# Performance work log

Measured on AMD Instinct MI355X. Metric: run time of the kernel, lower is better.

The kernel has to match this reference:

```python
import jax, jax.numpy as jnp
import numpy as np

B, S, T, D_IN = 32, 64, 30, 500  # batch, outer seq, LSTM time steps, LSTM input size
L = 64  # stacked LSTM layers, hidden_size = 1


def setup_inputs() -> dict:
    key = jax.random.key(0)
    ks = jax.random.split(key, 9)
    s = 0.2  # param scale ~ uniform(-1,1) stddev regime of torch init (1/sqrt(hidden)=1)
    return {
        "x": jax.random.normal(ks[0], (B, S, T * D_IN), jnp.float32),
        "w_ih0": jax.random.normal(ks[1], (4, D_IN), jnp.float32) * s,
        "w_hh0": jax.random.normal(ks[2], (4, 1), jnp.float32) * s,
        "b_ih0": jax.random.normal(ks[3], (4,), jnp.float32) * s,
        "b_hh0": jax.random.normal(ks[4], (4,), jnp.float32) * s,
        "w_ih": jax.random.normal(ks[5], (L - 1, 4, 1), jnp.float32) * s,
        "w_hh": jax.random.normal(ks[6], (L - 1, 4, 1), jnp.float32) * s,
        "b_ih": jax.random.normal(ks[7], (L - 1, 4), jnp.float32) * s,
        "b_hh": jax.random.normal(ks[8], (L - 1, 4), jnp.float32) * s,
    }


def _scan_layer(pre, whh):
    """Run one hidden-width-1 LSTM layer. pre: (T, N, 4) input-side gate preacts
    (incl. both biases); whh: (4,) recurrent weights. Returns hidden stream (T, N)."""
    N = pre.shape[1]
    z = jnp.zeros((N,), pre.dtype)

    def cell(carry, g_in):
        h, c = carry
        g = g_in + h[:, None] * whh  # (N, 4), torch gate order i,f,g,o
        i = jax.nn.sigmoid(g[:, 0])
        f = jax.nn.sigmoid(g[:, 1])
        gg = jnp.tanh(g[:, 2])
        o = jax.nn.sigmoid(g[:, 3])
        c = f * c + i * gg
        h = o * jnp.tanh(c)
        return (h, c), h

    _, hs = jax.lax.scan(cell, (z, z), pre)
    return hs  # (T, N)


def reference(x, w_ih0, w_hh0, b_ih0, b_hh0, w_ih, w_hh, b_ih, b_hh):
    b, s, d = x.shape
    xf = jnp.flip(x, -1).reshape(b * s, T, D_IN)  # (N, T, 500)
    # layer 0: precompute input contribution for all timesteps (the only GEMM)
    pre0 = jnp.einsum('ntd,gd->tng', xf, w_ih0) + b_ih0 + b_hh0  # (T, N, 4)
    hs = _scan_layer(pre0, w_hh0[:, 0])  # (T, N)

    # layers 1..63: scalar-input LSTMs, scanned over the layer axis
    def layer_step(seq, params):
        wih, whh, bias = params  # (4,), (4,), (4,)
        pre = seq[:, :, None] * wih + bias  # (T, N, 4)
        return _scan_layer(pre, whh), None

    hs, _ = jax.lax.scan(layer_step, hs, (w_ih[:, :, 0], w_hh[:, :, 0], b_ih + b_hh))
    return hs.transpose(1, 0).reshape(b, s, T)  # (B, S, 30)
```

## Files before the change

### kernel.cpp

```cpp
#include <hip/hip_runtime.h>

#define NSEQ 2048
#define TT 30
#define DIN 500
#define NLAYER 64

__device__ __forceinline__ float fexp(float x) {
    return __builtin_amdgcn_exp2f(x * 1.4426950408889634f);
}
__device__ __forceinline__ float fsigmoid(float x) {
    return __builtin_amdgcn_rcpf(1.0f + fexp(-x));
}
__device__ __forceinline__ float ftanh_(float x) {
    return fmaf(-2.0f, __builtin_amdgcn_rcpf(1.0f + fexp(2.0f * x)), 1.0f);
}
__device__ __forceinline__ float rdlane(float v, int l) {
    return __builtin_bit_cast(float, __builtin_amdgcn_readlane(__builtin_bit_cast(int, v), l));
}
template <int CTRL>
__device__ __forceinline__ float dppmv(float v) {
    return __builtin_bit_cast(float, __builtin_amdgcn_update_dpp(
        0, __builtin_bit_cast(int, v), CTRL, 0xF, 0xF, false));
}
#define DPP_XOR1 0xB1
#define DPP_XOR2 0x4E
#define DPP_ROR4 0x124
#define DPP_ROR8 0x128
#define DPP_SHR1 0x138

__device__ __forceinline__ float dot4rev(const float4 xv, const float4 wv, float acc) {
    acc = fmaf(xv.x, wv.w, acc);
    acc = fmaf(xv.y, wv.z, acc);
    acc = fmaf(xv.z, wv.y, acc);
    acc = fmaf(xv.w, wv.x, acc);
    return acc;
}
__device__ __forceinline__ float red16(float a) {
    a += dppmv<DPP_XOR1>(a);
    a += dppmv<DPP_XOR2>(a);
    a += dppmv<DPP_ROR4>(a);
    a += dppmv<DPP_ROR8>(a);
    return a;
}

__global__ __launch_bounds__(256, 2) void fused_lstm(
    const float* __restrict__ x,
    const float* __restrict__ w_ih0,
    const float* __restrict__ w_hh0,
    const float* __restrict__ b_ih0,
    const float* __restrict__ b_hh0,
    const float* __restrict__ w_ih,
    const float* __restrict__ w_hh,
    const float* __restrict__ b_ih,
    const float* __restrict__ b_hh,
    float* __restrict__ out)
{
    __shared__ float pre[4][TT * 4];

    const int tid  = threadIdx.x;
    const int lane = tid & 63;
    const int w    = tid >> 6;
    const int n    = blockIdx.x * 4 + w;
    const int s    = lane & 15;
    const int g    = lane >> 4;
    float* __restrict__ prew = pre[w];

    const int l = (lane == 0) ? 0 : (lane - 1);
    float4 wihv  = *(const float4*)(w_ih + l * 4);
    float4 whhv  = *(const float4*)(w_hh + l * 4);
    float4 bihv  = *(const float4*)(b_ih + l * 4);
    float4 bhhv  = *(const float4*)(b_hh + l * 4);
    float4 whh0v = *(const float4*)(w_hh0);
    float4 bi0v  = *(const float4*)(b_ih0);
    float4 bh0v  = *(const float4*)(b_hh0);
    __builtin_amdgcn_sched_barrier(0);

    const float4* __restrict__ w4 = (const float4*)w_ih0;
    const float4 z4 = make_float4(0.f, 0.f, 0.f, 0.f);
    float4 wk[4][8];
#pragma unroll
    for (int gate = 0; gate < 4; ++gate) {
#pragma unroll
        for (int k = 0; k < 8; ++k) {
            const int j = k * 16 + s;
            wk[gate][k] = (j < 125) ? w4[gate * 125 + (124 - j)] : z4;
        }
    }

    const float4* __restrict__ xq = (const float4*)(x + (size_t)n * (TT * DIN));
    auto xround = [&](int r, float4 (&b)[8]) {
        const int t = r * 4 + g;
        int cc = TT - 1 - t; if (cc < 0) cc = 0;
        const float4* __restrict__ p = xq + cc * 125;
#pragma unroll
        for (int k = 0; k < 8; ++k) {
            const int j = k * 16 + s;
            b[k] = p[(j < 125) ? j : 124];
        }
    };
    auto cround = [&](const float4 (&b)[8], int r) {
        float a0 = 0.f, a1 = 0.f, a2 = 0.f, a3 = 0.f;
#pragma unroll
        for (int k = 0; k < 8; ++k) {
            a0 = dot4rev(b[k], wk[0][k], a0);
            a1 = dot4rev(b[k], wk[1][k], a1);
            a2 = dot4rev(b[k], wk[2][k], a2);
            a3 = dot4rev(b[k], wk[3][k], a3);
        }
        a0 = red16(a0); a1 = red16(a1); a2 = red16(a2); a3 = red16(a3);
        const int t = r * 4 + g;
        if (s == 0 && t < TT)
            *(float4*)&prew[t * 4] = make_float4(a0, a1, a2, a3);
    };

    float4 A[8], B[8];
    xround(0, A);
#pragma unroll
    for (int r = 0; r < 8; r += 2) {
        if (r + 1 < 8) xround(r + 1, B);
        __builtin_amdgcn_sched_barrier(0);
        cround(A, r);
        if (r + 2 < 8) xround(r + 2, A);
        __builtin_amdgcn_sched_barrier(0);
        cround(B, r + 1);
    }
    asm volatile("s_waitcnt lgkmcnt(0)" ::: "memory");

    float wih0, wih1, wih2, wih3, whh0, whh1, whh2, whh3;
    float bia0, bia1, bia2, bia3;
    if (lane == 0) {
        wih0 = wih1 = wih2 = wih3 = 0.f;
        bia0 = bia1 = bia2 = bia3 = 0.f;
        whh0 = whh0v.x; whh1 = whh0v.y; whh2 = whh0v.z; whh3 = whh0v.w;
    } else {
        wih0 = wihv.x; wih1 = wihv.y; wih2 = wihv.z; wih3 = wihv.w;
        whh0 = whhv.x; whh1 = whhv.y; whh2 = whhv.z; whh3 = whhv.w;
        bia0 = bihv.x + bhhv.x; bia1 = bihv.y + bhhv.y;
        bia2 = bihv.z + bhhv.z; bia3 = bihv.w + bhhv.w;
    }
    float pg0 = 0.f, pg1 = 0.f, pg2 = 0.f, pg3 = 0.f;
    if (lane < TT) {
        const float4 q = *(const float4*)&prew[lane * 4];
        pg0 = q.x + bi0v.x + bh0v.x;
        pg1 = q.y + bi0v.y + bh0v.y;
        pg2 = q.z + bi0v.z + bh0v.z;
        pg3 = q.w + bi0v.w + bh0v.w;
    }

    float h = 0.f, c = 0.f;
    for (int k = 0; k < NLAYER + TT - 1; ++k) {
        const float h_in = dppmv<DPP_SHR1>(h);
        const int t = k - lane;
        const bool active = (t >= 0) && (t < TT);

        float g0, g1, g2, g3;
        if (lane == 0) {
            g0 = g1 = g2 = g3 = 0.f;
        } else {
            g0 = fmaf(h_in, wih0, bia0);
            g1 = fmaf(h_in, wih1, bia1);
            g2 = fmaf(h_in, wih2, bia2);
            g3 = fmaf(h_in, wih3, bia3);
        }
        if (k < TT) {
            const float p0 = rdlane(pg0, k);
            const float p1 = rdlane(pg1, k);
            const float p2 = rdlane(pg2, k);
            const float p3 = rdlane(pg3, k);
            if (lane == 0) { g0 = p0; g1 = p1; g2 = p2; g3 = p3; }
        }
        g0 = fmaf(h, whh0, g0);
        g1 = fmaf(h, whh1, g1);
        g2 = fmaf(h, whh2, g2);
        g3 = fmaf(h, whh3, g3);

        const float ig = fsigmoid(g0);
        const float fg = fsigmoid(g1);
        const float gg = ftanh_(g2);
        const float og = fsigmoid(g3);
        const float cn = fmaf(fg, c, ig * gg);
        const float hn = og * ftanh_(cn);

        if (active) { c = cn; h = hn; }
        if (lane == 63 && active) out[(size_t)n * TT + t] = hn;
    }
}

extern "C" void kernel_launch(void* const* d_in, const int* in_sizes, int n_in,
                              void* d_out, int out_size, void* d_ws, size_t ws_size,
                              hipStream_t stream) {
    const float* x     = (const float*)d_in[0];
    const float* w_ih0 = (const float*)d_in[1];
    const float* w_hh0 = (const float*)d_in[2];
    const float* b_ih0 = (const float*)d_in[3];
    const float* b_hh0 = (const float*)d_in[4];
    const float* w_ih  = (const float*)d_in[5];
    const float* w_hh  = (const float*)d_in[6];
    const float* b_ih  = (const float*)d_in[7];
    const float* b_hh  = (const float*)d_in[8];
    float* out = (float*)d_out;

    fused_lstm<<<NSEQ / 4, 256, 0, stream>>>(x, w_ih0, w_hh0, b_ih0, b_hh0,
                                             w_ih, w_hh, b_ih, b_hh, out);
}
```

Baseline: 42.11 us.

## Split fused LSTM into separate GEMV kernel and recurrence kernel via workspace

Splits the fused kernel in two. The first kernel computes the layer-0 input projection with one block per sequence: each wave covers 8 timesteps, holds weights in fewer registers, uses a full-wave DPP reduction, and can run more blocks per CU. Its gate preactivations go to a global workspace, and a second kernel reads them back for the wavefront-skewed recurrence. This gives the memory-bound GEMV more parallelism and frees the recurrence kernel from holding weight registers, at the cost of an extra launch and a global write/read round trip.

```diff
diff --git a/kernel.cpp b/kernel.cpp
--- a/kernel.cpp
+++ b/kernel.cpp
@@ -22,11 +22,13 @@
     return __builtin_bit_cast(float, __builtin_amdgcn_update_dpp(
         0, __builtin_bit_cast(int, v), CTRL, 0xF, 0xF, false));
 }
-#define DPP_XOR1 0xB1
-#define DPP_XOR2 0x4E
-#define DPP_ROR4 0x124
-#define DPP_ROR8 0x128
-#define DPP_SHR1 0x138
+#define DPP_ROW_SHR1   0x111
+#define DPP_ROW_SHR2   0x112
+#define DPP_ROW_SHR4   0x114
+#define DPP_ROW_SHR8   0x118
+#define DPP_BCAST15    0x142
+#define DPP_BCAST31    0x143
+#define DPP_SHR1       0x138
 
 __device__ __forceinline__ float dot4rev(const float4 xv, const float4 wv, float acc) {
     acc = fmaf(xv.x, wv.w, acc);
@@ -35,17 +37,68 @@
     acc = fmaf(xv.w, wv.x, acc);
     return acc;
 }
-__device__ __forceinline__ float red16(float a) {
-    a += dppmv<DPP_XOR1>(a);
-    a += dppmv<DPP_XOR2>(a);
-    a += dppmv<DPP_ROR4>(a);
-    a += dppmv<DPP_ROR8>(a);
+__device__ __forceinline__ float red64(float a) {
+    a += dppmv<DPP_ROW_SHR1>(a);
+    a += dppmv<DPP_ROW_SHR2>(a);
+    a += dppmv<DPP_ROW_SHR4>(a);
+    a += dppmv<DPP_ROW_SHR8>(a);
+    a += dppmv<DPP_BCAST15>(a);
+    a += dppmv<DPP_BCAST31>(a);
     return a;
 }
 
-__global__ __launch_bounds__(256, 2) void fused_lstm(
+__global__ __launch_bounds__(256, 4) void lstm_gemv(
     const float* __restrict__ x,
     const float* __restrict__ w_ih0,
+    float4* __restrict__ preg)
+{
+    const int tid  = threadIdx.x;
+    const int lane = tid & 63;
+    const int w    = tid >> 6;
+    const int n    = blockIdx.x;
+
+    const float4* __restrict__ w4 = (const float4*)w_ih0;
+    const float4 z4 = make_float4(0.f, 0.f, 0.f, 0.f);
+    float4 wq0[4], wq1[4];
+#pragma unroll
+    for (int g = 0; g < 4; ++g) {
+        wq0[g] = w4[g * 125 + (124 - lane)];
+        wq1[g] = (lane < 61) ? w4[g * 125 + (60 - lane)] : z4;
+    }
+
+    const float4* __restrict__ xq = (const float4*)(x + (size_t)n * (TT * DIN));
+    const int xb_idx = (lane < 61) ? (64 + lane) : 124;
+
+    float4 xa[8], xb[8];
+    auto issue = [&](int i) {
+        const int t = 8 * w + i;
+        if (t < TT) {
+            const float4* __restrict__ p = xq + (TT - 1 - t) * 125;
+            xa[i] = p[lane];
+            xb[i] = p[xb_idx];
+        }
+    };
+    issue(0); issue(1); issue(2);
+    __builtin_amdgcn_sched_barrier(0);
+#pragma unroll
+    for (int i = 0; i < 8; ++i) {
+        if (i + 3 < 8) issue(i + 3);
+        __builtin_amdgcn_sched_barrier(0);
+        const int t = 8 * w + i;
+        if (t < TT) {
+            float a0 = dot4rev(xa[i], wq0[0], 0.f); a0 = dot4rev(xb[i], wq1[0], a0);
+            float a1 = dot4rev(xa[i], wq0[1], 0.f); a1 = dot4rev(xb[i], wq1[1], a1);
+            float a2 = dot4rev(xa[i], wq0[2], 0.f); a2 = dot4rev(xb[i], wq1[2], a2);
+            float a3 = dot4rev(xa[i], wq0[3], 0.f); a3 = dot4rev(xb[i], wq1[3], a3);
+            a0 = red64(a0); a1 = red64(a1); a2 = red64(a2); a3 = red64(a3);
+            if (lane == 63) preg[n * TT + t] = make_float4(a0, a1, a2, a3);
+        }
+        __builtin_amdgcn_sched_barrier(0);
+    }
+}
+
+__global__ __launch_bounds__(256, 2) void lstm_rec(
+    const float4* __restrict__ preg,
     const float* __restrict__ w_hh0,
     const float* __restrict__ b_ih0,
     const float* __restrict__ b_hh0,
@@ -55,76 +108,19 @@
     const float* __restrict__ b_hh,
     float* __restrict__ out)
 {
-    __shared__ float pre[4][TT * 4];
-
     const int tid  = threadIdx.x;
     const int lane = tid & 63;
     const int w    = tid >> 6;
     const int n    = blockIdx.x * 4 + w;
-    const int s    = lane & 15;
-    const int g    = lane >> 4;
-    float* __restrict__ prew = pre[w];
 
     const int l = (lane == 0) ? 0 : (lane - 1);
-    float4 wihv  = *(const float4*)(w_ih + l * 4);
-    float4 whhv  = *(const float4*)(w_hh + l * 4);
-    float4 bihv  = *(const float4*)(b_ih + l * 4);
-    float4 bhhv  = *(const float4*)(b_hh + l * 4);
-    float4 whh0v = *(const float4*)(w_hh0);
-    float4 bi0v  = *(const float4*)(b_ih0);
-    float4 bh0v  = *(const float4*)(b_hh0);
-    __builtin_amdgcn_sched_barrier(0);
-
-    const float4* __restrict__ w4 = (const float4*)w_ih0;
-    const float4 z4 = make_float4(0.f, 0.f, 0.f, 0.f);
-    float4 wk[4][8];
-#pragma unroll
-    for (int gate = 0; gate < 4; ++gate) {
-#pragma unroll
-        for (int k = 0; k < 8; ++k) {
-            const int j = k * 16 + s;
-            wk[gate][k] = (j < 125) ? w4[gate * 125 + (124 - j)] : z4;
-        }
-    }
-
-    const float4* __restrict__ xq = (const float4*)(x + (size_t)n * (TT * DIN));
-    auto xround = [&](int r, float4 (&b)[8]) {
-        const int t = r * 4 + g;
-        int cc = TT - 1 - t; if (cc < 0) cc = 0;
-        const float4* __restrict__ p = xq + cc * 125;
-#pragma unroll
-        for (int k = 0; k < 8; ++k) {
-            const int j = k * 16 + s;
-            b[k] = p[(j < 125) ? j : 124];
-        }
-    };
-    auto cround = [&](const float4 (&b)[8], int r) {
-        float a0 = 0.f, a1 = 0.f, a2 = 0.f, a3 = 0.f;
-#pragma unroll
-        for (int k = 0; k < 8; ++k) {
-            a0 = dot4rev(b[k], wk[0][k], a0);
-            a1 = dot4rev(b[k], wk[1][k], a1);
-            a2 = dot4rev(b[k], wk[2][k], a2);
-            a3 = dot4rev(b[k], wk[3][k], a3);
-        }
-        a0 = red16(a0); a1 = red16(a1); a2 = red16(a2); a3 = red16(a3);
-        const int t = r * 4 + g;
-        if (s == 0 && t < TT)
-            *(float4*)&prew[t * 4] = make_float4(a0, a1, a2, a3);
-    };
-
-    float4 A[8], B[8];
-    xround(0, A);
-#pragma unroll
-    for (int r = 0; r < 8; r += 2) {
-        if (r + 1 < 8) xround(r + 1, B);
-        __builtin_amdgcn_sched_barrier(0);
-        cround(A, r);
-        if (r + 2 < 8) xround(r + 2, A);
-        __builtin_amdgcn_sched_barrier(0);
-        cround(B, r + 1);
-    }
-    asm volatile("s_waitcnt lgkmcnt(0)" ::: "memory");
+    const float4 wihv  = *(const float4*)(w_ih + l * 4);
+    const float4 whhv  = *(const float4*)(w_hh + l * 4);
+    const float4 bihv  = *(const float4*)(b_ih + l * 4);
+    const float4 bhhv  = *(const float4*)(b_hh + l * 4);
+    const float4 whh0v = *(const float4*)(w_hh0);
+    const float4 bi0v  = *(const float4*)(b_ih0);
+    const float4 bh0v  = *(const float4*)(b_hh0);
 
     float wih0, wih1, wih2, wih3, whh0, whh1, whh2, whh3;
     float bia0, bia1, bia2, bia3;
@@ -140,7 +136,7 @@
     }
     float pg0 = 0.f, pg1 = 0.f, pg2 = 0.f, pg3 = 0.f;
     if (lane < TT) {
-        const float4 q = *(const float4*)&prew[lane * 4];
+        const float4 q = preg[n * TT + lane];
         pg0 = q.x + bi0v.x + bh0v.x;
         pg1 = q.y + bi0v.y + bh0v.y;
         pg2 = q.z + bi0v.z + bh0v.z;
@@ -200,6 +196,9 @@
     const float* b_hh  = (const float*)d_in[8];
     float* out = (float*)d_out;
 
-    fused_lstm<<<NSEQ / 4, 256, 0, stream>>>(x, w_ih0, w_hh0, b_ih0, b_hh0,
-                                             w_ih, w_hh, b_ih, b_hh, out);
-}
+    float4* preg = (float4*)d_ws;
+
+    lstm_gemv<<<NSEQ, 256, 0, stream>>>(x, w_ih0, preg);
+    lstm_rec<<<NSEQ / 4, 256, 0, stream>>>(preg, w_hh0, b_ih0, b_hh0,
+                                           w_ih, w_hh, b_ih, b_hh, out);
+}
```

Measured after the change: 52.84 us. 25.5% more time.
